# Kernel tuning notes

Hardware: AMD Instinct MI355X
Metric: run time of the kernel (lower is better)

The kernel has to match this reference:

```python
import math
import jax, jax.numpy as jnp
import numpy as np

B, C_IN, C_OUT, K, STYLE, H, W = 16, 512, 512, 3, 512, 64, 64


def setup_inputs() -> dict:
    key = jax.random.key(0)
    k1, k2, k3, k4 = jax.random.split(key, 4)
    return {
        "x": jax.random.normal(k1, (B, C_IN, H, W), jnp.float32),
        "style": jax.random.normal(k2, (B, STYLE), jnp.float32),
        "weight": jax.random.normal(k3, (C_OUT, C_IN, K, K), jnp.float32),  # learned conv weight (leading 1 dim of torch param squeezed)
        "mod_w": jax.random.normal(k4, (C_IN, STYLE), jnp.float32),         # EqualLinear weight
        "mod_b": jnp.ones((C_IN,), jnp.float32),                             # EqualLinear bias (bias_init=1)
    }


def reference(x, style, weight, mod_w, mod_b):
    # EqualLinear modulation: scale = 1/sqrt(style_dim), lr_mul = 1
    mod_scale = 1.0 / math.sqrt(STYLE)
    s = style @ (mod_w.T * mod_scale) + mod_b            # [B, C_IN]

    # per-sample modulated weight
    w_scale = 1.0 / math.sqrt(C_IN * K * K)
    w = w_scale * weight[None] * s[:, None, :, None, None]  # [B, C_OUT, C_IN, K, K]

    # demodulate
    demod = jax.lax.rsqrt(jnp.sum(w * w, axis=(2, 3, 4)) + 1e-8)  # [B, C_OUT]
    w = w * demod[:, :, None, None, None]

    pad = K // 2

    def conv_one(xi, wi):
        # xi: [C_IN, H, W], wi: [C_OUT, C_IN, K, K]
        return jax.lax.conv_general_dilated(
            xi[None], wi, window_strides=(1, 1),
            padding=[(pad, pad), (pad, pad)],
            dimension_numbers=("NCHW", "OIHW", "NCHW"),
        )[0]

    return jax.vmap(conv_one)(x, w)  # [B, C_OUT, H, W]
```

## Files before the change

kernel.cpp:

```cpp
#include <hip/hip_runtime.h>
#include <hip/hip_bf16.h>
#include <math.h>
#include <stdint.h>

#define B_     16
#define CI_    512
#define CO_    512
#define HH     64
#define WW     64
#define STYLE_ 512

typedef __bf16 bf16x8 __attribute__((ext_vector_type(8)));
typedef float f32x4 __attribute__((ext_vector_type(4)));

#define WS_S     0
#define WS_DEMOD 32768
#define WS_WSQ   65536
#define WS_WB    1114112
#define WS_XS    5832704

__device__ __forceinline__ void gload16(const void* g, void* l) {
    __builtin_amdgcn_global_load_lds((const __attribute__((address_space(1))) uint32_t*)g,
                                     (__attribute__((address_space(3))) uint32_t*)l, 16, 0, 0);
}

__global__ void k_style(const float* __restrict__ style, const float* __restrict__ mod_w,
                        const float* __restrict__ mod_b, float* __restrict__ s_out) {
    int b  = blockIdx.x;
    int ci = threadIdx.x;
    const float scale = 0.044194173824159216f;
    float acc = 0.f;
    const float* st = style + b * STYLE_;
    const float* mw = mod_w + (size_t)ci * STYLE_;
    for (int j = 0; j < STYLE_; ++j) acc += st[j] * mw[j];
    s_out[b * CI_ + ci] = acc * scale + mod_b[ci];
}

__global__ __launch_bounds__(256) void k_wprep(const float* __restrict__ weight,
                                               float* __restrict__ wsq, __bf16* __restrict__ wb) {
    int p = blockIdx.x * 256 + threadIdx.x;
    int co = p >> 9, ci = p & 511;
    const float* wp = weight + (size_t)p * 9;
    float acc = 0.f;
    #pragma unroll
    for (int t = 0; t < 9; ++t) {
        float v = wp[t];
        acc += v * v;
        wb[((((size_t)(ci >> 5) * 9 + t) * CO_) + co) * 32 + (ci & 31)] = (__bf16)v;
    }
    wsq[(size_t)ci * CO_ + co] = acc;
}

__global__ void k_demod(const float* __restrict__ s, const float* __restrict__ wsq,
                        float* __restrict__ demod) {
    int b = blockIdx.x, co = threadIdx.x;
    const float w_scale2 = 1.0f / 4608.0f;
    float acc = 0.f;
    const float* sb = s + b * CI_;
    for (int ci = 0; ci < CI_; ++ci) { float sv = sb[ci]; acc += sv * sv * wsq[(size_t)ci * CO_ + co]; }
    demod[b * CO_ + co] = 1.0f / sqrtf(acc * w_scale2 + 1e-8f);
}

__global__ __launch_bounds__(256) void k_xs(const float* __restrict__ x, const float* __restrict__ s,
                                            __bf16* __restrict__ xs) {
    __shared__ float Lt[64][65];
    const int y = blockIdx.x, b = blockIdx.y;
    const int tid = threadIdx.x;
    const float w_scale = 0.014731391274719739f;
    for (int ci0 = 0; ci0 < CI_; ci0 += 64) {
        for (int i = tid; i < 64 * 16; i += 256) {
            int ci = i >> 4, x4 = (i & 15) * 4;
            const float4 v = *(const float4*)&x[((size_t)(b * CI_ + ci0 + ci) * HH + y) * WW + x4];
            float sc = s[b * CI_ + ci0 + ci] * w_scale;
            Lt[ci][x4]     = v.x * sc;
            Lt[ci][x4 + 1] = v.y * sc;
            Lt[ci][x4 + 2] = v.z * sc;
            Lt[ci][x4 + 3] = v.w * sc;
        }
        __syncthreads();
        for (int o = tid; o < 512; o += 256) {
            int xx = o >> 3, oct = o & 7;
            int cb = ci0 + oct * 8;
            bf16x8 v;
            #pragma unroll
            for (int j = 0; j < 8; ++j) v[j] = (__bf16)Lt[oct * 8 + j][xx];
            size_t idx = ((((size_t)(cb >> 5) * 16 + b) * 66 + (y + 1)) * 64 + xx) * 32 + (cb & 31);
            *(bf16x8*)&xs[idx] = v;
        }
        __syncthreads();
    }
    if (y == 0 || y == 63) {
        const int row = (y == 0) ? 0 : 65;
        uint32_t* xs32 = (uint32_t*)xs;
        for (int c = 0; c < 16; ++c)
            for (int i = tid; i < 1024; i += 256)
                xs32[(((size_t)c * 16 + b) * 66 + row) * 1024 + i] = 0;
    }
}

#define XB 42240
#define WB 36864

__global__ __launch_bounds__(512, 1) void k_conv(
    const __bf16* __restrict__ xs, const __bf16* __restrict__ wb,
    const float* __restrict__ demod, float* __restrict__ out)
{
    __shared__ __align__(128) char smem[2 * XB + 2 * WB];

    const int tid  = threadIdx.x;
    const int lane = tid & 63;
    const int wave = tid >> 6;

    const int bid  = blockIdx.x;
    const int r8   = bid & 7;
    const int q    = bid >> 3;
    const int co0  = (q & 7) * 64;
    const int pair = (q >> 3) | (r8 << 4);
    const int y0   = (pair & 7) * 8;
    const int b    = pair >> 3;

    const int m  = lane & 15;
    const int g  = lane >> 4;
    const int qA = g ^ ((m >> 1) & 3);

    for (int i = tid; i < 640; i += 512) {
        int dw = i & 15, h = i >> 4;
        int buf = h / 20, hh = h % 20;
        int rr = hh >> 1, side = hh & 1;
        ((uint32_t*)smem)[buf * (XB / 4) + (rr * 66 + side * 65) * 16 + dw] = 0;
    }
    asm volatile("s_waitcnt lgkmcnt(0)" ::: "memory");

    uint32_t soff[10];
    uint32_t sdst[10];
    const __bf16* sb;
    size_t sstride;
    uint32_t selstride;
    if (wave < 4) {
        sb = xs + (size_t)b * (66 * 64 * 32);
        sstride = (size_t)16 * 66 * 64 * 32;
        selstride = XB;
        #pragma unroll
        for (int i = 0; i < 10; ++i) {
            int o = wave * 10 + i, r = o >> 2, seg = o & 3;
            int p = seg * 64 + lane;
            int xr = 1 + (p >> 2), qd = p & 3;
            int rowg = r * 66 + xr;
            int sq = qd ^ ((rowg >> 1) & 3);
            soff[i] = (uint32_t)(((y0 + r) * 64 + (xr - 1)) * 32 + sq * 8);
            sdst[i] = (uint32_t)((r * 66 + 1) * 64 + seg * 1024);
        }
    } else {
        sb = wb;
        sstride = (size_t)9 * CO_ * 32;
        selstride = WB;
        #pragma unroll
        for (int i = 0; i < 9; ++i) {
            int j = (wave - 4) * 9 + i;
            int p = j * 64 + lane;
            int row = p >> 2, qd = p & 3;
            int sq = qd ^ ((row >> 1) & 3);
            soff[i] = (uint32_t)(((row >> 6) * CO_ + co0 + (row & 63)) * 32 + sq * 8);
            sdst[i] = (uint32_t)(2 * XB + j * 1024);
        }
        soff[9] = 0; sdst[9] = 2 * XB;
    }

    uint32_t bbase[9];
    #pragma unroll
    for (int kh = 0; kh < 3; ++kh)
        #pragma unroll
        for (int kw = 0; kw < 3; ++kw) {
            int R = (wave + kh) * 66 + m + kw;
            int qB = g ^ ((R >> 1) & 3);
            bbase[kh * 3 + kw] = (uint32_t)(R * 64 + qB * 16);
        }
    const uint32_t abase = (uint32_t)(m * 64 + qA * 16);

    f32x4 acc[4][4];
    #pragma unroll
    for (int mi = 0; mi < 4; ++mi)
        #pragma unroll
        for (int nt = 0; nt < 4; ++nt) acc[mi][nt] = (f32x4){0.f, 0.f, 0.f, 0.f};

    auto stage = [&](const __bf16* base, int sel) {
        uint32_t so = sel * selstride;
        if (wave < 4) {
            #pragma unroll
            for (int i = 0; i < 10; ++i) gload16(base + soff[i], smem + so + sdst[i]);
        } else {
            #pragma unroll
            for (int i = 0; i < 9; ++i) gload16(base + soff[i], smem + so + sdst[i]);
        }
    };

    stage(sb, 0);

    for (int t = 0; t < 16; ++t) {
        if (t < 15) {
            sb += sstride;
            stage(sb, (t + 1) & 1);
            if (wave < 4) asm volatile("s_waitcnt vmcnt(10)" ::: "memory");
            else          asm volatile("s_waitcnt vmcnt(9)"  ::: "memory");
        } else {
            asm volatile("s_waitcnt vmcnt(0)" ::: "memory");
        }
        __builtin_amdgcn_s_barrier();

        const char* xbuf = smem + (t & 1) * XB;
        const char* wbuf = smem + 2 * XB + (t & 1) * WB + abase;

        __builtin_amdgcn_s_setprio(1);
        #pragma unroll
        for (int tp = 0; tp < 9; ++tp) {
            bf16x8 a0 = *(const bf16x8*)(wbuf + tp * 4096);
            bf16x8 a1 = *(const bf16x8*)(wbuf + tp * 4096 + 1024);
            bf16x8 a2 = *(const bf16x8*)(wbuf + tp * 4096 + 2048);
            bf16x8 a3 = *(const bf16x8*)(wbuf + tp * 4096 + 3072);
            #pragma unroll
            for (int nt = 0; nt < 4; ++nt) {
                bf16x8 bv = *(const bf16x8*)(xbuf + bbase[tp] + nt * 1024);
                acc[0][nt] = __builtin_amdgcn_mfma_f32_16x16x32_bf16(a0, bv, acc[0][nt], 0, 0, 0);
                acc[1][nt] = __builtin_amdgcn_mfma_f32_16x16x32_bf16(a1, bv, acc[1][nt], 0, 0, 0);
                acc[2][nt] = __builtin_amdgcn_mfma_f32_16x16x32_bf16(a2, bv, acc[2][nt], 0, 0, 0);
                acc[3][nt] = __builtin_amdgcn_mfma_f32_16x16x32_bf16(a3, bv, acc[3][nt], 0, 0, 0);
            }
        }
        __builtin_amdgcn_s_setprio(0);
        __builtin_amdgcn_s_barrier();
    }

    const int y = y0 + wave;
    #pragma unroll
    for (int mi = 0; mi < 4; ++mi) {
        #pragma unroll
        for (int j = 0; j < 4; ++j) {
            const int co = co0 + mi * 16 + g * 4 + j;
            const float dm = demod[b * CO_ + co];
            float* op = out + ((size_t)(b * CO_ + co) * HH + y) * WW;
            #pragma unroll
            for (int nt = 0; nt < 4; ++nt)
                op[nt * 16 + m] = acc[mi][nt][j] * dm;
        }
    }
}

extern "C" void kernel_launch(void* const* d_in, const int* in_sizes, int n_in,
                              void* d_out, int out_size, void* d_ws, size_t ws_size,
                              hipStream_t stream) {
    const float* x      = (const float*)d_in[0];
    const float* style  = (const float*)d_in[1];
    const float* weight = (const float*)d_in[2];
    const float* mod_w  = (const float*)d_in[3];
    const float* mod_b  = (const float*)d_in[4];
    float* out = (float*)d_out;

    char* wsb = (char*)d_ws;
    float*  s_buf = (float*)(wsb + WS_S);
    float*  demod = (float*)(wsb + WS_DEMOD);
    float*  wsq   = (float*)(wsb + WS_WSQ);
    __bf16* wb    = (__bf16*)(wsb + WS_WB);
    __bf16* xs    = (__bf16*)(wsb + WS_XS);

    k_style<<<dim3(B_), dim3(CI_), 0, stream>>>(style, mod_w, mod_b, s_buf);
    k_wprep<<<dim3(CO_ * CI_ / 256), dim3(256), 0, stream>>>(weight, wsq, wb);
    k_demod<<<dim3(B_), dim3(CO_), 0, stream>>>(s_buf, wsq, demod);
    k_xs<<<dim3(HH, B_), dim3(256), 0, stream>>>(x, s_buf, xs);
    k_conv<<<dim3(1024), dim3(512), 0, stream>>>(xs, wb, demod, out);
}
```

Before: 339.2 us.

## Switch conv to 32x32x16 MFMA with 128-channel tiles and 16-channel chunks

```diff
diff --git a/kernel.cpp b/kernel.cpp
--- a/kernel.cpp
+++ b/kernel.cpp
@@ -11,7 +11,7 @@
 #define STYLE_ 512
 
 typedef __bf16 bf16x8 __attribute__((ext_vector_type(8)));
-typedef float f32x4 __attribute__((ext_vector_type(4)));
+typedef float f32x16 __attribute__((ext_vector_type(16)));
 
 #define WS_S     0
 #define WS_DEMOD 32768
@@ -41,12 +41,13 @@
     int p = blockIdx.x * 256 + threadIdx.x;
     int co = p >> 9, ci = p & 511;
     const float* wp = weight + (size_t)p * 9;
+    const int slot = (((ci >> 3) & 1) ^ ((co >> 2) & 1));
     float acc = 0.f;
     #pragma unroll
     for (int t = 0; t < 9; ++t) {
         float v = wp[t];
         acc += v * v;
-        wb[((((size_t)(ci >> 5) * 9 + t) * CO_) + co) * 32 + (ci & 31)] = (__bf16)v;
+        wb[((((size_t)(ci >> 4) * 9 + t) * CO_) + co) * 16 + slot * 8 + (ci & 7)] = (__bf16)v;
     }
     wsq[(size_t)ci * CO_ + co] = acc;
 }
@@ -81,10 +82,12 @@
         for (int o = tid; o < 512; o += 256) {
             int xx = o >> 3, oct = o & 7;
             int cb = ci0 + oct * 8;
+            int chunk = cb >> 4;
+            int slot = (oct & 1) ^ (((xx + 1) >> 2) & 1);
             bf16x8 v;
             #pragma unroll
             for (int j = 0; j < 8; ++j) v[j] = (__bf16)Lt[oct * 8 + j][xx];
-            size_t idx = ((((size_t)(cb >> 5) * 16 + b) * 66 + (y + 1)) * 64 + xx) * 32 + (cb & 31);
+            size_t idx = (((size_t)chunk * 16 + b) * 66 + (y + 1)) * 1024 + xx * 16 + slot * 8;
             *(bf16x8*)&xs[idx] = v;
         }
         __syncthreads();
@@ -92,13 +95,13 @@
     if (y == 0 || y == 63) {
         const int row = (y == 0) ? 0 : 65;
         uint32_t* xs32 = (uint32_t*)xs;
-        for (int c = 0; c < 16; ++c)
-            for (int i = tid; i < 1024; i += 256)
-                xs32[(((size_t)c * 16 + b) * 66 + row) * 1024 + i] = 0;
-    }
-}
-
-#define XB 42240
+        for (int c = 0; c < 32; ++c)
+            for (int i = tid; i < 512; i += 256)
+                xs32[(((size_t)c * 16 + b) * 66 + row) * 512 + i] = 0;
+    }
+}
+
+#define XB 21120
 #define WB 36864
 
 __global__ __launch_bounds__(512, 1) void k_conv(
@@ -114,94 +117,80 @@
     const int bid  = blockIdx.x;
     const int r8   = bid & 7;
     const int q    = bid >> 3;
-    const int co0  = (q & 7) * 64;
-    const int pair = (q >> 3) | (r8 << 4);
-    const int y0   = (pair & 7) * 8;
-    const int b    = pair >> 3;
-
-    const int m  = lane & 15;
-    const int g  = lane >> 4;
-    const int qA = g ^ ((m >> 1) & 3);
-
-    for (int i = tid; i < 640; i += 512) {
-        int dw = i & 15, h = i >> 4;
-        int buf = h / 20, hh = h % 20;
-        int rr = hh >> 1, side = hh & 1;
-        ((uint32_t*)smem)[buf * (XB / 4) + (rr * 66 + side * 65) * 16 + dw] = 0;
+    const int co0  = (q & 3) * 128;
+    const int yb   = (q >> 2) | (r8 << 4);
+    const int y0   = (yb & 7) * 8;
+    const int b    = yb >> 3;
+
+    const int lm = lane & 31;
+    const int g2 = lane >> 5;
+
+    if (tid < 320) {
+        int buf = tid / 160, rem = tid % 160;
+        int rb = rem >> 4, hh = rem & 15;
+        int side = hh >> 3, dw = hh & 7;
+        ((uint32_t*)smem)[buf * (XB / 4) + rb * 528 + side * 520 + dw] = 0;
     }
     asm volatile("s_waitcnt lgkmcnt(0)" ::: "memory");
 
-    uint32_t soff[10];
-    uint32_t sdst[10];
-    const __bf16* sb;
-    size_t sstride;
-    uint32_t selstride;
+    uint32_t soff[9];
+    uint32_t sdst[9];
     if (wave < 4) {
-        sb = xs + (size_t)b * (66 * 64 * 32);
-        sstride = (size_t)16 * 66 * 64 * 32;
-        selstride = XB;
-        #pragma unroll
-        for (int i = 0; i < 10; ++i) {
-            int o = wave * 10 + i, r = o >> 2, seg = o & 3;
-            int p = seg * 64 + lane;
-            int xr = 1 + (p >> 2), qd = p & 3;
-            int rowg = r * 66 + xr;
-            int sq = qd ^ ((rowg >> 1) & 3);
-            soff[i] = (uint32_t)(((y0 + r) * 64 + (xr - 1)) * 32 + sq * 8);
-            sdst[i] = (uint32_t)((r * 66 + 1) * 64 + seg * 1024);
+        #pragma unroll
+        for (int i = 0; i < 5; ++i) {
+            int j = wave * 5 + i, rb = j >> 1, seg = j & 1;
+            soff[i] = (uint32_t)((y0 + rb) * 1024 + seg * 512 + lane * 8);
+            sdst[i] = (uint32_t)(rb * 2112 + 32 + seg * 1024 + lane * 16);
         }
     } else {
-        sb = wb;
-        sstride = (size_t)9 * CO_ * 32;
-        selstride = WB;
         #pragma unroll
         for (int i = 0; i < 9; ++i) {
             int j = (wave - 4) * 9 + i;
-            int p = j * 64 + lane;
-            int row = p >> 2, qd = p & 3;
-            int sq = qd ^ ((row >> 1) & 3);
-            soff[i] = (uint32_t)(((row >> 6) * CO_ + co0 + (row & 63)) * 32 + sq * 8);
-            sdst[i] = (uint32_t)(2 * XB + j * 1024);
-        }
-        soff[9] = 0; sdst[9] = 2 * XB;
-    }
-
+            int tap = j >> 2, seg = j & 3;
+            soff[i] = (uint32_t)(tap * 8192 + co0 * 16 + seg * 512 + lane * 8);
+            sdst[i] = (uint32_t)(j * 1024 + lane * 16);
+        }
+    }
+
+    const uint32_t aq    = (uint32_t)(g2 ^ ((lm >> 2) & 1));
+    const uint32_t abase = (uint32_t)(lm * 32 + aq * 16);
     uint32_t bbase[9];
     #pragma unroll
     for (int kh = 0; kh < 3; ++kh)
         #pragma unroll
         for (int kw = 0; kw < 3; ++kw) {
-            int R = (wave + kh) * 66 + m + kw;
-            int qB = g ^ ((R >> 1) & 3);
-            bbase[kh * 3 + kw] = (uint32_t)(R * 64 + qB * 16);
-        }
-    const uint32_t abase = (uint32_t)(m * 64 + qA * 16);
-
-    f32x4 acc[4][4];
+            int xr0 = lm + kw;
+            int qb  = g2 ^ ((xr0 >> 2) & 1);
+            bbase[kh * 3 + kw] = (uint32_t)((wave + kh) * 2112 + xr0 * 32 + qb * 16);
+        }
+
+    f32x16 acc[4][2];
     #pragma unroll
     for (int mi = 0; mi < 4; ++mi)
         #pragma unroll
-        for (int nt = 0; nt < 4; ++nt) acc[mi][nt] = (f32x4){0.f, 0.f, 0.f, 0.f};
-
-    auto stage = [&](const __bf16* base, int sel) {
-        uint32_t so = sel * selstride;
+        for (int nt = 0; nt < 2; ++nt)
+            #pragma unroll
+            for (int r = 0; r < 16; ++r) acc[mi][nt][r] = 0.f;
+
+    auto stage = [&](int chunk, int sel) {
         if (wave < 4) {
-            #pragma unroll
-            for (int i = 0; i < 10; ++i) gload16(base + soff[i], smem + so + sdst[i]);
+            const __bf16* base = xs + (size_t)chunk * 1081344 + (size_t)b * 67584;
+            #pragma unroll
+            for (int i = 0; i < 5; ++i) gload16(base + soff[i], smem + sel * XB + sdst[i]);
         } else {
-            #pragma unroll
-            for (int i = 0; i < 9; ++i) gload16(base + soff[i], smem + so + sdst[i]);
+            const __bf16* base = wb + (size_t)chunk * 73728;
+            #pragma unroll
+            for (int i = 0; i < 9; ++i) gload16(base + soff[i], smem + 2 * XB + sel * WB + sdst[i]);
         }
     };
 
-    stage(sb, 0);
-
-    for (int t = 0; t < 16; ++t) {
-        if (t < 15) {
-            sb += sstride;
-            stage(sb, (t + 1) & 1);
-            if (wave < 4) asm volatile("s_waitcnt vmcnt(10)" ::: "memory");
-            else          asm volatile("s_waitcnt vmcnt(9)"  ::: "memory");
+    stage(0, 0);
+
+    for (int t = 0; t < 32; ++t) {
+        if (t < 31) {
+            stage(t + 1, (t + 1) & 1);
+            if (wave < 4) asm volatile("s_waitcnt vmcnt(5)" ::: "memory");
+            else          asm volatile("s_waitcnt vmcnt(9)" ::: "memory");
         } else {
             asm volatile("s_waitcnt vmcnt(0)" ::: "memory");
         }
@@ -213,17 +202,18 @@
         __builtin_amdgcn_s_setprio(1);
         #pragma unroll
         for (int tp = 0; tp < 9; ++tp) {
-            bf16x8 a0 = *(const bf16x8*)(wbuf + tp * 4096);
-            bf16x8 a1 = *(const bf16x8*)(wbuf + tp * 4096 + 1024);
-            bf16x8 a2 = *(const bf16x8*)(wbuf + tp * 4096 + 2048);
-            bf16x8 a3 = *(const bf16x8*)(wbuf + tp * 4096 + 3072);
-            #pragma unroll
-            for (int nt = 0; nt < 4; ++nt) {
+            const char* wp = wbuf + tp * 4096;
+            bf16x8 a0 = *(const bf16x8*)(wp);
+            bf16x8 a1 = *(const bf16x8*)(wp + 1024);
+            bf16x8 a2 = *(const bf16x8*)(wp + 2048);
+            bf16x8 a3 = *(const bf16x8*)(wp + 3072);
+            #pragma unroll
+            for (int nt = 0; nt < 2; ++nt) {
                 bf16x8 bv = *(const bf16x8*)(xbuf + bbase[tp] + nt * 1024);
-                acc[0][nt] = __builtin_amdgcn_mfma_f32_16x16x32_bf16(a0, bv, acc[0][nt], 0, 0, 0);
-                acc[1][nt] = __builtin_amdgcn_mfma_f32_16x16x32_bf16(a1, bv, acc[1][nt], 0, 0, 0);
-                acc[2][nt] = __builtin_amdgcn_mfma_f32_16x16x32_bf16(a2, bv, acc[2][nt], 0, 0, 0);
-                acc[3][nt] = __builtin_amdgcn_mfma_f32_16x16x32_bf16(a3, bv, acc[3][nt], 0, 0, 0);
+                acc[0][nt] = __builtin_amdgcn_mfma_f32_32x32x16_bf16(a0, bv, acc[0][nt], 0, 0, 0);
+                acc[1][nt] = __builtin_amdgcn_mfma_f32_32x32x16_bf16(a1, bv, acc[1][nt], 0, 0, 0);
+                acc[2][nt] = __builtin_amdgcn_mfma_f32_32x32x16_bf16(a2, bv, acc[2][nt], 0, 0, 0);
+                acc[3][nt] = __builtin_amdgcn_mfma_f32_32x32x16_bf16(a3, bv, acc[3][nt], 0, 0, 0);
             }
         }
         __builtin_amdgcn_s_setprio(0);
@@ -231,16 +221,15 @@
     }
 
     const int y = y0 + wave;
+    float* outb = out + (size_t)b * CO_ * 4096 + (size_t)y * 64;
     #pragma unroll
     for (int mi = 0; mi < 4; ++mi) {
         #pragma unroll
-        for (int j = 0; j < 4; ++j) {
-            const int co = co0 + mi * 16 + g * 4 + j;
+        for (int reg = 0; reg < 16; ++reg) {
+            const int co = co0 + mi * 32 + (reg & 3) + 8 * (reg >> 2) + 4 * g2;
             const float dm = demod[b * CO_ + co];
-            float* op = out + ((size_t)(b * CO_ + co) * HH + y) * WW;
-            #pragma unroll
-            for (int nt = 0; nt < 4; ++nt)
-                op[nt * 16 + m] = acc[mi][nt][j] * dm;
+            outb[(size_t)co * 4096 + lm]      = acc[mi][0][reg] * dm;
+            outb[(size_t)co * 4096 + 32 + lm] = acc[mi][1][reg] * dm;
         }
     }
 }
@@ -266,5 +255,5 @@
     k_wprep<<<dim3(CO_ * CI_ / 256), dim3(256), 0, stream>>>(weight, wsq, wb);
     k_demod<<<dim3(B_), dim3(CO_), 0, stream>>>(s_buf, wsq, demod);
     k_xs<<<dim3(HH, B_), dim3(256), 0, stream>>>(x, s_buf, xs);
-    k_conv<<<dim3(1024), dim3(512), 0, stream>>>(xs, wb, demod, out);
-}
+    k_conv<<<dim3(512), dim3(512), 0, stream>>>(xs, wb, demod, out);
+}
```

Result: slower. 356.0 us (+4.9%).
